# Kernel optimization log

Hardware: AMD Instinct MI355X
Metric: run time of the kernel (lower is better)

The kernel has to match this reference:

```python
import jax, jax.numpy as jnp
import numpy as np

B, T, M, P = 64, 2048, 512, 512


def setup_inputs() -> dict:
    key = jax.random.key(0)
    ks = jax.random.split(key, 9)
    s = 0.02
    return {
        "hidden_state": jax.random.normal(ks[0], (B, P), jnp.float32),
        "cell_state": jax.random.normal(ks[1], (B, P), jnp.float32),
        "encoder_h": jax.random.normal(ks[2], (B, T, M), jnp.float32),
        # Dense W_d: (2p -> m)
        "W_d": jax.random.normal(ks[3], (2 * P, M), jnp.float32) * s,
        "b_wd": jnp.zeros((M,), jnp.float32),
        # Dense U_d: (m -> m)
        "U_d": jax.random.normal(ks[4], (M, M), jnp.float32) * s,
        "b_ud": jnp.zeros((M,), jnp.float32),
        # Dense v_d: (m -> 1)
        "v_d": jax.random.normal(ks[5], (M, 1), jnp.float32) * s,
        "b_vd": jnp.zeros((1,), jnp.float32),
    }


def reference(hidden_state, cell_state, encoder_h, W_d, b_wd, U_d, b_ud, v_d, b_vd):
    # W_d(RepeatVector(T)(concat([d, s]))): the Dense is applied to the same
    # (B, 2p) vector at every time step, so compute it once and broadcast.
    ds = jnp.concatenate([hidden_state, cell_state], axis=-1)          # (B, 2p)
    ds_proj = ds @ W_d + b_wd                                          # (B, m)
    enc_proj = jnp.einsum('btm,mn->btn', encoder_h, U_d) + b_ud        # (B, T, m)
    e = jnp.tanh(ds_proj[:, None, :] + enc_proj)                       # (B, T, m)
    l = e @ v_d + b_vd                                                 # (B, T, 1)
    return jax.nn.softmax(l, axis=1)                                   # softmax over T
```

## Files before the change

### kernel.cpp

```cpp
#include <hip/hip_runtime.h>
#include <cstdint>
#include <cstddef>


typedef float  floatx4 __attribute__((ext_vector_type(4)));
typedef short  shortx8 __attribute__((ext_vector_type(8)));

__device__ __forceinline__ short f2bf_rne(float f) {
  unsigned u = __float_as_uint(f);
  unsigned r = u + 0x7FFFu + ((u >> 16) & 1u);
  return (short)(r >> 16);
}

__device__ __forceinline__ unsigned pack_bf_trunc(float lo, float hi) {
  return __builtin_amdgcn_perm(__float_as_uint(hi), __float_as_uint(lo), 0x07060302u);
}

#define GLOAD_LDS16(gptr, lptr)                                                 \
  __builtin_amdgcn_global_load_lds(                                             \
      (const __attribute__((address_space(1))) void*)(gptr),                    \
      (__attribute__((address_space(3))) void*)(lptr), 16, 0, 0)

#define SB() __builtin_amdgcn_sched_barrier(0)
#define WAIT_VM(n) asm volatile("s_waitcnt vmcnt(" #n ")" ::: "memory")
#define WAIT_LGKM0() asm volatile("s_waitcnt lgkmcnt(0)" ::: "memory")

extern "C" __global__ __launch_bounds__(256) void prep_kernel(
    const float* __restrict__ hidden, const float* __restrict__ cell,
    const float* __restrict__ W_d, const float* __restrict__ b_wd,
    const float* __restrict__ U_d, const float* __restrict__ b_ud,
    float* __restrict__ S, short* __restrict__ UT, float* __restrict__ lzero)
{
  int bx = blockIdx.x, tid = threadIdx.x;
  if (bx < 128) {
    int idx = bx * 256 + tid;
    int b = idx >> 9, n = idx & 511;
    const float* h = hidden + b * 512;
    const float* c = cell   + b * 512;
    float acc = b_wd[n] + b_ud[n];
    for (int k = 0; k < 512; ++k) acc = fmaf(h[k], W_d[k * 512 + n], acc);
    for (int k = 0; k < 512; ++k) acc = fmaf(c[k], W_d[(k + 512) * 512 + n], acc);
    S[idx] = acc;
  } else if (bx < 384) {
    int idx = (bx - 128) * 1024 + tid * 4;
    int cbp = idx >> 17;
    int r2  = idx & 131071;
    int ktp = r2 >> 13;
    int sI  = r2 & 8191;
    int n    = sI >> 5;
    int slot = (sI >> 3) & 3;
    int b16  = sI & 7;
    int kb16 = slot ^ (n & 3);
    int k0 = ktp * 32 + (kb16 << 3) + b16;
    int ng = cbp * 256 + n;
    unsigned lo = (unsigned short)f2bf_rne(U_d[(size_t)(k0 + 0) * 512 + ng]) |
                  ((unsigned)(unsigned short)f2bf_rne(U_d[(size_t)(k0 + 1) * 512 + ng]) << 16);
    unsigned hi = (unsigned short)f2bf_rne(U_d[(size_t)(k0 + 2) * 512 + ng]) |
                  ((unsigned)(unsigned short)f2bf_rne(U_d[(size_t)(k0 + 3) * 512 + ng]) << 16);
    uint2 w; w.x = lo; w.y = hi;
    *(uint2*)(UT + idx) = w;
  } else {
    int idx = ((bx - 384) * 256 + tid) * 4;
    floatx4 z = {0.f, 0.f, 0.f, 0.f};
    *(floatx4*)(lzero + idx) = z;
  }
}

extern "C" __global__ __launch_bounds__(512, 2) void attn_gemm(
    const float* __restrict__ A, const short* __restrict__ UT,
    const float* __restrict__ S, const float* __restrict__ vd,
    float* __restrict__ lout)
{
  __shared__ short As[2][8192];
  __shared__ short Bs[2][8192];

  const int tid = threadIdx.x;
  const int bx  = blockIdx.x;
  const int xcd = bx & 7;
  const int wg  = xcd * 128 + (bx >> 3);
  const int cb  = wg & 1;
  const int rb  = wg >> 1;
  const int row0 = rb << 8;
  const int col0 = cb << 8;
  const int wave = tid >> 6;
  const int lane = tid & 63;
  const int wr = wave >> 2, wc = wave & 3;
  const int q = lane >> 4, l15 = lane & 15;

  const float* asrc[4];
  int awr[4];
#pragma unroll
  for (int j = 0; j < 4; ++j) {
    int row = j * 64 + (tid >> 3);
    int ch  = tid & 7;
    asrc[j] = A + (size_t)(row0 + row) * 512 + ch * 4;
    awr[j]  = row * 32 + ((((ch >> 1) ^ (row & 3)) << 3) + (ch & 1) * 4);
  }
  const short* bsrc[2];
  int bdst[2];
#pragma unroll
  for (int j = 0; j < 2; ++j) {
    int ws = j * 8 + wave;
    bsrc[j] = UT + cb * 131072 + ws * 512 + lane * 8;
    bdst[j] = ws * 512;
  }

  int aoff[8], boff[4];
#pragma unroll
  for (int tr = 0; tr < 8; ++tr) {
    int row = wr * 128 + tr * 16 + l15;
    aoff[tr] = row * 32 + ((q ^ (row & 3)) << 3);
  }
#pragma unroll
  for (int tc = 0; tc < 4; ++tc) {
    int n = wc * 64 + tc * 16 + l15;
    boff[tc] = n * 32 + ((q ^ (n & 3)) << 3);
  }

  floatx4 acc[8][4];
#pragma unroll
  for (int i = 0; i < 8; ++i)
#pragma unroll
    for (int j = 0; j < 4; ++j)
      acc[i][j] = (floatx4){0.f, 0.f, 0.f, 0.f};

  floatx4 areg[4];

#pragma unroll
  for (int j = 0; j < 4; ++j) areg[j] = *(const floatx4*)(asrc[j]);
  SB();
#pragma unroll
  for (int j = 0; j < 2; ++j) GLOAD_LDS16(bsrc[j], &Bs[0][bdst[j]]);
  SB();
  WAIT_VM(2); SB();
#pragma unroll
  for (int j = 0; j < 4; ++j) {
    uint2 w;
    w.x = pack_bf_trunc(areg[j].x, areg[j].y);
    w.y = pack_bf_trunc(areg[j].z, areg[j].w);
    *(uint2*)(&As[0][0] + awr[j]) = w;
  }
  SB();
#pragma unroll
  for (int j = 0; j < 4; ++j) areg[j] = *(const floatx4*)(asrc[j] + 32);
  SB();
  WAIT_VM(4); SB();
  WAIT_LGKM0(); SB();
  __builtin_amdgcn_s_barrier(); SB();

#pragma unroll
  for (int t = 0; t < 16; ++t) {
    const int cur = t & 1;
    const short* Ab = &As[cur][0];
    const short* Bb = &Bs[cur][0];
    shortx8 af[4], bfr[4];
#pragma unroll
    for (int tc = 0; tc < 4; ++tc) bfr[tc] = *(const shortx8*)(Bb + boff[tc]);
#pragma unroll
    for (int tr = 0; tr < 4; ++tr) af[tr] = *(const shortx8*)(Ab + aoff[tr]);
    WAIT_LGKM0(); SB();
    __builtin_amdgcn_s_setprio(1);
#pragma unroll
    for (int tr = 0; tr < 4; ++tr)
#pragma unroll
      for (int tc = 0; tc < 4; ++tc)
        acc[tr][tc] = __builtin_amdgcn_mfma_f32_16x16x32_bf16(
            af[tr], bfr[tc], acc[tr][tc], 0, 0, 0);
    __builtin_amdgcn_s_setprio(0);
    SB();
    if (t < 15) {
      WAIT_VM(0); SB();
      short* An = &As[cur ^ 1][0];
#pragma unroll
      for (int j = 0; j < 4; ++j) {
        uint2 w;
        w.x = pack_bf_trunc(areg[j].x, areg[j].y);
        w.y = pack_bf_trunc(areg[j].z, areg[j].w);
        *(uint2*)(An + awr[j]) = w;
      }
#pragma unroll
      for (int j = 0; j < 2; ++j)
        GLOAD_LDS16(bsrc[j] + (t + 1) * 8192, &Bs[cur ^ 1][bdst[j]]);
      SB();
      if (t < 14) {
#pragma unroll
        for (int j = 0; j < 4; ++j)
          areg[j] = *(const floatx4*)(asrc[j] + (t + 2) * 32);
      }
      SB();
    }
#pragma unroll
    for (int tr = 0; tr < 4; ++tr) af[tr] = *(const shortx8*)(Ab + aoff[tr + 4]);
    WAIT_LGKM0(); SB();
    __builtin_amdgcn_s_setprio(1);
#pragma unroll
    for (int tr = 0; tr < 4; ++tr)
#pragma unroll
      for (int tc = 0; tc < 4; ++tc)
        acc[tr + 4][tc] = __builtin_amdgcn_mfma_f32_16x16x32_bf16(
            af[tr], bfr[tc], acc[tr + 4][tc], 0, 0, 0);
    __builtin_amdgcn_s_setprio(0);
    SB();
    if (t < 15) {
      if (t < 14) { WAIT_VM(4); }
      else        { WAIT_VM(0); }
      SB();
      __builtin_amdgcn_s_barrier();
      SB();
    }
  }

  const int bb = rb >> 3;
  const float* Srow = S + bb * 512;
  float sv[4], vv[4];
#pragma unroll
  for (int tc = 0; tc < 4; ++tc) {
    int n = col0 + wc * 64 + tc * 16 + l15;
    sv[tc] = Srow[n];
    vv[tc] = vd[n];
  }
#pragma unroll
  for (int tr = 0; tr < 8; ++tr) {
#pragma unroll
    for (int r = 0; r < 4; ++r) {
      float ssum = 0.f;
#pragma unroll
      for (int tc = 0; tc < 4; ++tc) {
        float x = acc[tr][tc][r] + sv[tc];
        x = fminf(15.f, fmaxf(-15.f, x));
        float e2 = __expf(2.f * x);
        float e = (e2 - 1.f) / (e2 + 1.f);
        ssum += e * vv[tc];
      }
      ssum += __shfl_xor(ssum, 1);
      ssum += __shfl_xor(ssum, 2);
      ssum += __shfl_xor(ssum, 4);
      ssum += __shfl_xor(ssum, 8);
      if (l15 == 0) {
        int row = row0 + wr * 128 + tr * 16 + q * 4 + r;
        atomicAdd(lout + row, ssum);
      }
    }
  }
}

extern "C" __global__ __launch_bounds__(256) void softmax_t(float* __restrict__ l)
{
  int b = blockIdx.x, tid = threadIdx.x;
  int wave = tid >> 6, lane = tid & 63;
  float* row = l + (size_t)b * 2048;
  float v[8];
  float mx = -3.4e38f;
#pragma unroll
  for (int i = 0; i < 8; ++i) { v[i] = row[tid + i * 256]; mx = fmaxf(mx, v[i]); }
#pragma unroll
  for (int m = 1; m < 64; m <<= 1) mx = fmaxf(mx, __shfl_xor(mx, m));
  __shared__ float red[8];
  if (lane == 0) red[wave] = mx;
  __syncthreads();
  mx = fmaxf(fmaxf(red[0], red[1]), fmaxf(red[2], red[3]));
  float s = 0.f;
#pragma unroll
  for (int i = 0; i < 8; ++i) { v[i] = __expf(v[i] - mx); s += v[i]; }
#pragma unroll
  for (int m = 1; m < 64; m <<= 1) s += __shfl_xor(s, m);
  if (lane == 0) red[4 + wave] = s;
  __syncthreads();
  s = red[4] + red[5] + red[6] + red[7];
  float inv = 1.f / s;
#pragma unroll
  for (int i = 0; i < 8; ++i) row[tid + i * 256] = v[i] * inv;
}

extern "C" void kernel_launch(void* const* d_in, const int* in_sizes, int n_in,
                              void* d_out, int out_size, void* d_ws, size_t ws_size,
                              hipStream_t stream) {
  const float* hidden = (const float*)d_in[0];
  const float* cell   = (const float*)d_in[1];
  const float* enc    = (const float*)d_in[2];
  const float* W_d    = (const float*)d_in[3];
  const float* b_wd   = (const float*)d_in[4];
  const float* U_d    = (const float*)d_in[5];
  const float* b_ud   = (const float*)d_in[6];
  const float* v_d    = (const float*)d_in[7];
  float* out = (float*)d_out;
  float* S   = (float*)d_ws;
  short* UT  = (short*)((char*)d_ws + 32768 * sizeof(float));

  hipLaunchKernelGGL(prep_kernel, dim3(512), dim3(256), 0, stream,
                     hidden, cell, W_d, b_wd, U_d, b_ud, S, UT, out);
  hipLaunchKernelGGL(attn_gemm, dim3(1024), dim3(512), 0, stream,
                     enc, UT, S, v_d, out);
  hipLaunchKernelGGL(softmax_t, dim3(64), dim3(256), 0, stream, out);
}
```

Baseline: 492.8 us.

## Double K-tile depth to 64 and split GEMM loop into four barrier-paced phases

The main GEMM now uses K-tiles of 64 instead of 32, which doubles the LDS buffers and halves the number of loop iterations. The swizzle layout of the prepacked U_d and of the A tile changes to 8-way XOR groups. Each iteration is split into four MFMA phases separated by workgroup barriers, with B global-to-LDS loads and A conversion stores interleaved between the phases, in a ping-pong style schedule. The prep kernel's dot-product loop also gets four independent accumulators. The extra barriers and the larger LDS footprint (64KB per block) may limit occupancy or add synchronisation stalls.

```diff
diff --git a/kernel.cpp b/kernel.cpp
--- a/kernel.cpp
+++ b/kernel.cpp
@@ -5,6 +5,7 @@
 
 typedef float  floatx4 __attribute__((ext_vector_type(4)));
 typedef short  shortx8 __attribute__((ext_vector_type(8)));
+typedef unsigned int uintx4 __attribute__((ext_vector_type(4)));
 
 __device__ __forceinline__ short f2bf_rne(float f) {
   unsigned u = __float_as_uint(f);
@@ -22,8 +23,11 @@
       (__attribute__((address_space(3))) void*)(lptr), 16, 0, 0)
 
 #define SB() __builtin_amdgcn_sched_barrier(0)
-#define WAIT_VM(n) asm volatile("s_waitcnt vmcnt(" #n ")" ::: "memory")
+#define WAIT_VM0() asm volatile("s_waitcnt vmcnt(0)" ::: "memory")
+#define WAIT_VM4() asm volatile("s_waitcnt vmcnt(4)" ::: "memory")
+#define WAIT_VM8() asm volatile("s_waitcnt vmcnt(8)" ::: "memory")
 #define WAIT_LGKM0() asm volatile("s_waitcnt lgkmcnt(0)" ::: "memory")
+#define BAR() __builtin_amdgcn_s_barrier()
 
 extern "C" __global__ __launch_bounds__(256) void prep_kernel(
     const float* __restrict__ hidden, const float* __restrict__ cell,
@@ -37,22 +41,31 @@
     int b = idx >> 9, n = idx & 511;
     const float* h = hidden + b * 512;
     const float* c = cell   + b * 512;
-    float acc = b_wd[n] + b_ud[n];
-    for (int k = 0; k < 512; ++k) acc = fmaf(h[k], W_d[k * 512 + n], acc);
-    for (int k = 0; k < 512; ++k) acc = fmaf(c[k], W_d[(k + 512) * 512 + n], acc);
-    S[idx] = acc;
+    float a0 = b_wd[n] + b_ud[n], a1 = 0.f, a2 = 0.f, a3 = 0.f;
+    for (int k = 0; k < 512; k += 4) {
+      a0 = fmaf(h[k + 0], W_d[(k + 0) * 512 + n], a0);
+      a1 = fmaf(h[k + 1], W_d[(k + 1) * 512 + n], a1);
+      a2 = fmaf(h[k + 2], W_d[(k + 2) * 512 + n], a2);
+      a3 = fmaf(h[k + 3], W_d[(k + 3) * 512 + n], a3);
+    }
+    for (int k = 0; k < 512; k += 4) {
+      a0 = fmaf(c[k + 0], W_d[(k + 512) * 512 + n], a0);
+      a1 = fmaf(c[k + 1], W_d[(k + 513) * 512 + n], a1);
+      a2 = fmaf(c[k + 2], W_d[(k + 514) * 512 + n], a2);
+      a3 = fmaf(c[k + 3], W_d[(k + 515) * 512 + n], a3);
+    }
+    S[idx] = (a0 + a1) + (a2 + a3);
   } else if (bx < 384) {
-    int idx = (bx - 128) * 1024 + tid * 4;
-    int cbp = idx >> 17;
-    int r2  = idx & 131071;
-    int ktp = r2 >> 13;
-    int sI  = r2 & 8191;
-    int n    = sI >> 5;
-    int slot = (sI >> 3) & 3;
-    int b16  = sI & 7;
-    int kb16 = slot ^ (n & 3);
-    int k0 = ktp * 32 + (kb16 << 3) + b16;
-    int ng = cbp * 256 + n;
+    int idx  = (bx - 128) * 1024 + tid * 4;
+    int tile = idx >> 14;
+    int cb = tile >> 3, kt = tile & 7;
+    int sI = idx & 16383;
+    int n  = sI >> 6;
+    int gp = (sI >> 3) & 7;
+    int bb = sI & 7;
+    int gl = gp ^ (n & 7);
+    int k0 = kt * 64 + gl * 8 + bb;
+    int ng = cb * 256 + n;
     unsigned lo = (unsigned short)f2bf_rne(U_d[(size_t)(k0 + 0) * 512 + ng]) |
                   ((unsigned)(unsigned short)f2bf_rne(U_d[(size_t)(k0 + 1) * 512 + ng]) << 16);
     unsigned hi = (unsigned short)f2bf_rne(U_d[(size_t)(k0 + 2) * 512 + ng]) |
@@ -71,8 +84,8 @@
     const float* __restrict__ S, const float* __restrict__ vd,
     float* __restrict__ lout)
 {
-  __shared__ short As[2][8192];
-  __shared__ short Bs[2][8192];
+  __shared__ short As[2][16384];
+  __shared__ short Bs[2][16384];
 
   const int tid = threadIdx.x;
   const int bx  = blockIdx.x;
@@ -87,35 +100,17 @@
   const int wr = wave >> 2, wc = wave & 3;
   const int q = lane >> 4, l15 = lane & 15;
 
-  const float* asrc[4];
-  int awr[4];
-#pragma unroll
-  for (int j = 0; j < 4; ++j) {
-    int row = j * 64 + (tid >> 3);
-    int ch  = tid & 7;
-    asrc[j] = A + (size_t)(row0 + row) * 512 + ch * 4;
-    awr[j]  = row * 32 + ((((ch >> 1) ^ (row & 3)) << 3) + (ch & 1) * 4);
-  }
-  const short* bsrc[2];
-  int bdst[2];
-#pragma unroll
-  for (int j = 0; j < 2; ++j) {
-    int ws = j * 8 + wave;
-    bsrc[j] = UT + cb * 131072 + ws * 512 + lane * 8;
-    bdst[j] = ws * 512;
-  }
-
-  int aoff[8], boff[4];
-#pragma unroll
-  for (int tr = 0; tr < 8; ++tr) {
-    int row = wr * 128 + tr * 16 + l15;
-    aoff[tr] = row * 32 + ((q ^ (row & 3)) << 3);
-  }
-#pragma unroll
-  for (int tc = 0; tc < 4; ++tc) {
-    int n = wc * 64 + tc * 16 + l15;
-    boff[tc] = n * 32 + ((q ^ (n & 3)) << 3);
-  }
+  const int arow = tid >> 1;
+  const int ah   = tid & 1;
+  const float* aptr = A + (size_t)(row0 + arow) * 512 + ah * 32;
+  const int awbase = arow * 64 + ((((ah * 4) ^ (arow & 7)) & 7) << 3);
+
+  const short* bptr = UT + (size_t)cb * 131072 + (wave * 4) * 512 + lane * 8;
+  const int bldsbase = wave * 2048;
+
+  const int fgp = (q ^ (l15 & 7)) << 3;
+  const int afrag0 = (wr * 128 + l15) * 64 + fgp;
+  const int bfrag0 = (wc * 64  + l15) * 64 + fgp;
 
   floatx4 acc[8][4];
 #pragma unroll
@@ -124,89 +119,152 @@
     for (int j = 0; j < 4; ++j)
       acc[i][j] = (floatx4){0.f, 0.f, 0.f, 0.f};
 
-  floatx4 areg[4];
-
-#pragma unroll
-  for (int j = 0; j < 4; ++j) areg[j] = *(const floatx4*)(asrc[j]);
-  SB();
-#pragma unroll
-  for (int j = 0; j < 2; ++j) GLOAD_LDS16(bsrc[j], &Bs[0][bdst[j]]);
-  SB();
-  WAIT_VM(2); SB();
-#pragma unroll
-  for (int j = 0; j < 4; ++j) {
-    uint2 w;
-    w.x = pack_bf_trunc(areg[j].x, areg[j].y);
-    w.y = pack_bf_trunc(areg[j].z, areg[j].w);
-    *(uint2*)(&As[0][0] + awr[j]) = w;
-  }
-  SB();
-#pragma unroll
-  for (int j = 0; j < 4; ++j) areg[j] = *(const floatx4*)(asrc[j] + 32);
-  SB();
-  WAIT_VM(4); SB();
+  floatx4 areg[8];
+
+  SB();
+#pragma unroll
+  for (int i = 0; i < 8; ++i) areg[i] = *(const floatx4*)(aptr + i * 4);
+  SB();
+#pragma unroll
+  for (int j = 0; j < 4; ++j)
+    GLOAD_LDS16(bptr + j * 512, &Bs[0][bldsbase + j * 512]);
+  SB();
+  WAIT_VM4(); SB();
+#pragma unroll
+  for (int gi = 0; gi < 4; ++gi) {
+    uintx4 w;
+    w.x = pack_bf_trunc(areg[2 * gi].x, areg[2 * gi].y);
+    w.y = pack_bf_trunc(areg[2 * gi].z, areg[2 * gi].w);
+    w.z = pack_bf_trunc(areg[2 * gi + 1].x, areg[2 * gi + 1].y);
+    w.w = pack_bf_trunc(areg[2 * gi + 1].z, areg[2 * gi + 1].w);
+    *(uintx4*)(&As[0][awbase ^ (gi * 8)]) = w;
+  }
+  SB();
+#pragma unroll
+  for (int i = 0; i < 8; ++i) areg[i] = *(const floatx4*)(aptr + 64 + i * 4);
+  SB();
+  WAIT_VM8(); SB();
   WAIT_LGKM0(); SB();
-  __builtin_amdgcn_s_barrier(); SB();
-
-#pragma unroll
-  for (int t = 0; t < 16; ++t) {
+  BAR(); SB();
+
+  shortx8 af[4][2], bfr[4][2];
+
+#pragma unroll 2
+  for (int t = 0; t < 8; ++t) {
     const int cur = t & 1;
     const short* Ab = &As[cur][0];
     const short* Bb = &Bs[cur][0];
-    shortx8 af[4], bfr[4];
-#pragma unroll
-    for (int tc = 0; tc < 4; ++tc) bfr[tc] = *(const shortx8*)(Bb + boff[tc]);
-#pragma unroll
-    for (int tr = 0; tr < 4; ++tr) af[tr] = *(const shortx8*)(Ab + aoff[tr]);
-    WAIT_LGKM0(); SB();
+    short* An = &As[cur ^ 1][0];
+    short* Bn = &Bs[cur ^ 1][0];
+    const short* bnext = bptr + (t + 1) * 16384;
+
+#pragma unroll
+    for (int tc = 0; tc < 2; ++tc)
+#pragma unroll
+      for (int s = 0; s < 2; ++s)
+        bfr[tc][s] = *(const shortx8*)(Bb + ((bfrag0 + tc * 1024) ^ (s * 32)));
+#pragma unroll
+    for (int tr = 0; tr < 4; ++tr)
+#pragma unroll
+      for (int s = 0; s < 2; ++s)
+        af[tr][s] = *(const shortx8*)(Ab + ((afrag0 + tr * 1024) ^ (s * 32)));
+    SB();
+    if (t < 7) {
+      GLOAD_LDS16(bnext,       Bn + bldsbase);
+      GLOAD_LDS16(bnext + 512, Bn + bldsbase + 512);
+    }
+    SB();
+    BAR(); WAIT_LGKM0(); SB();
     __builtin_amdgcn_s_setprio(1);
 #pragma unroll
     for (int tr = 0; tr < 4; ++tr)
 #pragma unroll
-      for (int tc = 0; tc < 4; ++tc)
-        acc[tr][tc] = __builtin_amdgcn_mfma_f32_16x16x32_bf16(
-            af[tr], bfr[tc], acc[tr][tc], 0, 0, 0);
+      for (int tc = 0; tc < 2; ++tc)
+#pragma unroll
+        for (int s = 0; s < 2; ++s)
+          acc[tr][tc] = __builtin_amdgcn_mfma_f32_16x16x32_bf16(
+              af[tr][s], bfr[tc][s], acc[tr][tc], 0, 0, 0);
     __builtin_amdgcn_s_setprio(0);
-    SB();
-    if (t < 15) {
-      WAIT_VM(0); SB();
-      short* An = &As[cur ^ 1][0];
-#pragma unroll
-      for (int j = 0; j < 4; ++j) {
-        uint2 w;
-        w.x = pack_bf_trunc(areg[j].x, areg[j].y);
-        w.y = pack_bf_trunc(areg[j].z, areg[j].w);
-        *(uint2*)(An + awr[j]) = w;
-      }
-#pragma unroll
-      for (int j = 0; j < 2; ++j)
-        GLOAD_LDS16(bsrc[j] + (t + 1) * 8192, &Bs[cur ^ 1][bdst[j]]);
-      SB();
-      if (t < 14) {
-#pragma unroll
-        for (int j = 0; j < 4; ++j)
-          areg[j] = *(const floatx4*)(asrc[j] + (t + 2) * 32);
+    SB(); BAR();
+
+#pragma unroll
+    for (int tc = 2; tc < 4; ++tc)
+#pragma unroll
+      for (int s = 0; s < 2; ++s)
+        bfr[tc][s] = *(const shortx8*)(Bb + ((bfrag0 + tc * 1024) ^ (s * 32)));
+    SB();
+    if (t < 7) {
+      GLOAD_LDS16(bnext + 1024, Bn + bldsbase + 1024);
+      GLOAD_LDS16(bnext + 1536, Bn + bldsbase + 1536);
+    }
+    SB();
+    BAR(); WAIT_LGKM0(); SB();
+    __builtin_amdgcn_s_setprio(1);
+#pragma unroll
+    for (int tr = 0; tr < 4; ++tr)
+#pragma unroll
+      for (int tc = 2; tc < 4; ++tc)
+#pragma unroll
+        for (int s = 0; s < 2; ++s)
+          acc[tr][tc] = __builtin_amdgcn_mfma_f32_16x16x32_bf16(
+              af[tr][s], bfr[tc][s], acc[tr][tc], 0, 0, 0);
+    __builtin_amdgcn_s_setprio(0);
+    SB(); BAR();
+
+    if (t < 7) {
+      WAIT_VM4(); SB();
+#pragma unroll
+      for (int gi = 0; gi < 4; ++gi) {
+        uintx4 w;
+        w.x = pack_bf_trunc(areg[2 * gi].x, areg[2 * gi].y);
+        w.y = pack_bf_trunc(areg[2 * gi].z, areg[2 * gi].w);
+        w.z = pack_bf_trunc(areg[2 * gi + 1].x, areg[2 * gi + 1].y);
+        w.w = pack_bf_trunc(areg[2 * gi + 1].z, areg[2 * gi + 1].w);
+        *(uintx4*)(An + (awbase ^ (gi * 8))) = w;
       }
       SB();
     }
 #pragma unroll
-    for (int tr = 0; tr < 4; ++tr) af[tr] = *(const shortx8*)(Ab + aoff[tr + 4]);
-    WAIT_LGKM0(); SB();
+    for (int tr = 0; tr < 4; ++tr)
+#pragma unroll
+      for (int s = 0; s < 2; ++s)
+        af[tr][s] = *(const shortx8*)(Ab + ((afrag0 + (tr + 4) * 1024) ^ (s * 32)));
+    SB();
+    if (t < 6) {
+#pragma unroll
+      for (int i = 0; i < 8; ++i)
+        areg[i] = *(const floatx4*)(aptr + (t + 2) * 64 + i * 4);
+    }
+    SB();
+    BAR(); WAIT_LGKM0(); SB();
     __builtin_amdgcn_s_setprio(1);
 #pragma unroll
     for (int tr = 0; tr < 4; ++tr)
 #pragma unroll
-      for (int tc = 0; tc < 4; ++tc)
-        acc[tr + 4][tc] = __builtin_amdgcn_mfma_f32_16x16x32_bf16(
-            af[tr], bfr[tc], acc[tr + 4][tc], 0, 0, 0);
+      for (int tc = 0; tc < 2; ++tc)
+#pragma unroll
+        for (int s = 0; s < 2; ++s)
+          acc[tr + 4][tc] = __builtin_amdgcn_mfma_f32_16x16x32_bf16(
+              af[tr][s], bfr[tc][s], acc[tr + 4][tc], 0, 0, 0);
     __builtin_amdgcn_s_setprio(0);
-    SB();
-    if (t < 15) {
-      if (t < 14) { WAIT_VM(4); }
-      else        { WAIT_VM(0); }
+    SB(); BAR();
+
+    __builtin_amdgcn_s_setprio(1);
+#pragma unroll
+    for (int tr = 0; tr < 4; ++tr)
+#pragma unroll
+      for (int tc = 2; tc < 4; ++tc)
+#pragma unroll
+        for (int s = 0; s < 2; ++s)
+          acc[tr + 4][tc] = __builtin_amdgcn_mfma_f32_16x16x32_bf16(
+              af[tr][s], bfr[tc][s], acc[tr + 4][tc], 0, 0, 0);
+    __builtin_amdgcn_s_setprio(0);
+    SB();
+    if (t < 7) {
+      if (t < 6) { WAIT_VM8(); }
+      else       { WAIT_VM0(); }
       SB();
-      __builtin_amdgcn_s_barrier();
-      SB();
+      BAR(); SB();
     }
   }
 
```

Result: slower. 506.7 us (+2.8%).
